# Kernel tuning notes

Measured on AMD Instinct MI355X. Metric: run time of the kernel, lower is better.

## Reference

```python
import jax, jax.numpy as jnp
import numpy as np

D_MODEL = 2048
N_HEADS = 16
HEAD_DIM = D_MODEL // N_HEADS
D_FF = 8192
B, T = 2, 2048
LN_EPS = 1e-5


def layer_norm(x, g, b):
    mu = jnp.mean(x, axis=-1, keepdims=True)
    var = jnp.mean(jnp.square(x - mu), axis=-1, keepdims=True)
    return (x - mu) * jax.lax.rsqrt(var + LN_EPS) * g + b


def setup_inputs() -> dict:
    key = jax.random.key(0)
    ks = jax.random.split(key, 8)
    s = 0.02
    return {
        "x": jax.random.normal(ks[0], (B, T, D_MODEL), dtype=jnp.float32),
        "ln1_g": jnp.ones((D_MODEL,), jnp.float32),
        "ln1_b": jnp.zeros((D_MODEL,), jnp.float32),
        "ln2_g": jnp.ones((D_MODEL,), jnp.float32),
        "ln2_b": jnp.zeros((D_MODEL,), jnp.float32),
        "w_qkv": jax.random.normal(ks[1], (3 * D_MODEL, D_MODEL), jnp.float32) * s,
        "w_out": jax.random.normal(ks[2], (D_MODEL, D_MODEL), jnp.float32) * s,
        "w_up": jax.random.normal(ks[3], (D_FF, D_MODEL), jnp.float32) * s,
        "b_up": jnp.zeros((D_FF,), jnp.float32),
        "w_down": jax.random.normal(ks[4], (D_MODEL, D_FF), jnp.float32) * s,
        "b_down": jnp.zeros((D_MODEL,), jnp.float32),
    }


def reference(x, ln1_g, ln1_b, ln2_g, ln2_b, w_qkv, w_out, w_up, b_up, w_down, b_down):
    b, t, c = x.shape
    # --- attention (pre-norm) ---
    h = layer_norm(x, ln1_g, ln1_b)
    qkv = h @ w_qkv.T                                  # [B,T,3C]
    q, k, v = jnp.split(qkv, 3, axis=-1)
    # [B,H,T,Dh]
    q = q.reshape(b, t, N_HEADS, HEAD_DIM).transpose(0, 2, 1, 3)
    k = k.reshape(b, t, N_HEADS, HEAD_DIM).transpose(0, 2, 1, 3)
    v = v.reshape(b, t, N_HEADS, HEAD_DIM).transpose(0, 2, 1, 3)
    scale = 1.0 / np.sqrt(HEAD_DIM).astype(np.float32)
    attn = jnp.einsum("bhqd,bhkd->bhqk", q, k) * scale
    causal = jnp.tril(jnp.ones((t, t), dtype=bool))
    attn = jnp.where(causal, attn, jnp.float32(-jnp.inf))
    attn = jax.nn.softmax(attn, axis=-1)
    out = jnp.einsum("bhqk,bhkd->bhqd", attn, v)
    out = out.transpose(0, 2, 1, 3).reshape(b, t, c)
    x = x + out @ w_out.T
    # --- FFN (pre-norm, GeLU exact) ---
    h = layer_norm(x, ln2_g, ln2_b)
    h = jax.nn.gelu(h @ w_up.T + b_up, approximate=False)
    x = x + h @ w_down.T + b_down
    return x
```

## Files before the change

kernel.cpp:

```cpp
#include <hip/hip_runtime.h>
#include <cstdint>
#include <cstddef>

using u16 = unsigned short;
typedef __attribute__((ext_vector_type(8))) __bf16 bf16x8;
typedef __attribute__((ext_vector_type(4))) float f32x4;

__device__ inline u16 f2bf(float f) {
  union { float f; unsigned u; } v; v.f = f;
  unsigned r = (v.u + 0x7fffu + ((v.u >> 16) & 1u)) >> 16;
  return (u16)r;
}

__device__ inline float bf2f(u16 u) {
  union { unsigned u; float f; } v; v.u = (unsigned)u << 16;
  return v.f;
}

#define GLDS(g, s) __builtin_amdgcn_global_load_lds( \
    (__attribute__((address_space(1))) void*)(g), \
    (__attribute__((address_space(3))) void*)(s), 16, 0, 0)

__global__ __launch_bounds__(256) void cvt_all(const float* __restrict__ a0,
                                               const float* __restrict__ a1,
                                               const float* __restrict__ a2,
                                               const float* __restrict__ a3,
                                               u16* __restrict__ o0, u16* __restrict__ o1,
                                               u16* __restrict__ o2, u16* __restrict__ o3) {
  int stride = gridDim.x * 256;
  for (int i = blockIdx.x * 256 + threadIdx.x; i < 6291456; i += stride) {
    const float* in; u16* out; int j = i;
    if (j < 1572864) { in = a0; out = o0; }
    else if ((j -= 1572864) < 524288) { in = a1; out = o1; }
    else if ((j -= 524288) < 2097152) { in = a2; out = o2; }
    else { j -= 2097152; in = a3; out = o3; }
    float4 v0 = *(const float4*)&in[(size_t)j * 8];
    float4 v1 = *(const float4*)&in[(size_t)j * 8 + 4];
    union { u16 u[8]; uint4 q; } pk;
    pk.u[0] = f2bf(v0.x); pk.u[1] = f2bf(v0.y); pk.u[2] = f2bf(v0.z); pk.u[3] = f2bf(v0.w);
    pk.u[4] = f2bf(v1.x); pk.u[5] = f2bf(v1.y); pk.u[6] = f2bf(v1.z); pk.u[7] = f2bf(v1.w);
    *(uint4*)&out[(size_t)j * 8] = pk.q;
  }
}

__global__ __launch_bounds__(256) void ln_bf16(const float* __restrict__ x,
                                               const float* __restrict__ g,
                                               const float* __restrict__ bsh,
                                               u16* __restrict__ out) {
  __shared__ float red[8];
  int tid = threadIdx.x;
  int lane = tid & 63, w = tid >> 6;
  size_t row = blockIdx.x;
  const float* xr = x + row * 2048;
  float4 v0 = *(const float4*)&xr[tid * 8];
  float4 v1 = *(const float4*)&xr[tid * 8 + 4];
  float s = v0.x + v0.y + v0.z + v0.w + v1.x + v1.y + v1.z + v1.w;
  float s2 = v0.x*v0.x + v0.y*v0.y + v0.z*v0.z + v0.w*v0.w
           + v1.x*v1.x + v1.y*v1.y + v1.z*v1.z + v1.w*v1.w;
#pragma unroll
  for (int m = 1; m < 64; m <<= 1) { s += __shfl_xor(s, m); s2 += __shfl_xor(s2, m); }
  if (lane == 0) { red[w] = s; red[w + 4] = s2; }
  __syncthreads();
  s = red[0] + red[1] + red[2] + red[3];
  s2 = red[4] + red[5] + red[6] + red[7];
  float mu = s * (1.0f / 2048.0f);
  float var = s2 * (1.0f / 2048.0f) - mu * mu;
  float rs = rsqrtf(var + 1e-5f);
  float4 g0 = *(const float4*)&g[tid * 8];
  float4 g1 = *(const float4*)&g[tid * 8 + 4];
  float4 b0 = *(const float4*)&bsh[tid * 8];
  float4 b1 = *(const float4*)&bsh[tid * 8 + 4];
  float xv[8] = {v0.x, v0.y, v0.z, v0.w, v1.x, v1.y, v1.z, v1.w};
  float gv[8] = {g0.x, g0.y, g0.z, g0.w, g1.x, g1.y, g1.z, g1.w};
  float bv[8] = {b0.x, b0.y, b0.z, b0.w, b1.x, b1.y, b1.z, b1.w};
  union { u16 u[8]; uint4 q; } pk;
#pragma unroll
  for (int j = 0; j < 8; j++) pk.u[j] = f2bf((xv[j] - mu) * rs * gv[j] + bv[j]);
  *(uint4*)&out[row * 2048 + tid * 8] = pk.q;
}

__global__ __launch_bounds__(256) void combineLN(const u16* __restrict__ p,
                                                 const float* __restrict__ resid,
                                                 const float* __restrict__ g,
                                                 const float* __restrict__ bsh,
                                                 float* __restrict__ x1,
                                                 u16* __restrict__ hb) {
  __shared__ float red[8];
  int tid = threadIdx.x, lane = tid & 63, w = tid >> 6;
  size_t row = blockIdx.x;
  size_t base = row * 2048 + tid * 8;
  union { uint4 q; u16 u[8]; } a, b;
  a.q = *(const uint4*)&p[base];
  b.q = *(const uint4*)&p[8388608 + base];
  float4 r0 = *(const float4*)&resid[base];
  float4 r1 = *(const float4*)&resid[base + 4];
  float v[8] = {r0.x, r0.y, r0.z, r0.w, r1.x, r1.y, r1.z, r1.w};
  float s = 0.f, s2 = 0.f;
#pragma unroll
  for (int j = 0; j < 8; ++j) {
    v[j] += bf2f(a.u[j]) + bf2f(b.u[j]);
    s += v[j]; s2 += v[j] * v[j];
  }
  *(float4*)&x1[base] = (float4){v[0], v[1], v[2], v[3]};
  *(float4*)&x1[base + 4] = (float4){v[4], v[5], v[6], v[7]};
#pragma unroll
  for (int m = 1; m < 64; m <<= 1) { s += __shfl_xor(s, m); s2 += __shfl_xor(s2, m); }
  if (lane == 0) { red[w] = s; red[w + 4] = s2; }
  __syncthreads();
  s = red[0] + red[1] + red[2] + red[3];
  s2 = red[4] + red[5] + red[6] + red[7];
  float mu = s * (1.0f / 2048.0f);
  float var = s2 * (1.0f / 2048.0f) - mu * mu;
  float rs = rsqrtf(var + 1e-5f);
  float4 g0 = *(const float4*)&g[tid * 8];
  float4 g1 = *(const float4*)&g[tid * 8 + 4];
  float4 b0 = *(const float4*)&bsh[tid * 8];
  float4 b1 = *(const float4*)&bsh[tid * 8 + 4];
  float gv[8] = {g0.x, g0.y, g0.z, g0.w, g1.x, g1.y, g1.z, g1.w};
  float bv[8] = {b0.x, b0.y, b0.z, b0.w, b1.x, b1.y, b1.z, b1.w};
  union { u16 u[8]; uint4 q; } pk;
#pragma unroll
  for (int j = 0; j < 8; j++) pk.u[j] = f2bf((v[j] - mu) * rs * gv[j] + bv[j]);
  *(uint4*)&hb[base] = pk.q;
}

__global__ __launch_bounds__(256) void combine2f(const u16* __restrict__ p,
                                                 const float* __restrict__ resid,
                                                 const float* __restrict__ bias,
                                                 float* __restrict__ out, int n8) {
  int stride = gridDim.x * 256;
  for (int i = blockIdx.x * 256 + threadIdx.x; i < n8; i += stride) {
    size_t base = (size_t)i * 8;
    union { uint4 q; u16 u[8]; } a, b;
    a.q = *(const uint4*)&p[base];
    b.q = *(const uint4*)&p[8388608 + base];
    float4 r0 = *(const float4*)&resid[base];
    float4 r1 = *(const float4*)&resid[base + 4];
    int col0 = (int)(base & 2047);
    float4 bb0 = *(const float4*)&bias[col0];
    float4 bb1 = *(const float4*)&bias[col0 + 4];
    float v[8] = {r0.x + bb0.x, r0.y + bb0.y, r0.z + bb0.z, r0.w + bb0.w,
                  r1.x + bb1.x, r1.y + bb1.y, r1.z + bb1.z, r1.w + bb1.w};
#pragma unroll
    for (int j = 0; j < 8; ++j) v[j] += bf2f(a.u[j]) + bf2f(b.u[j]);
    *(float4*)&out[base] = (float4){v[0], v[1], v[2], v[3]};
    *(float4*)&out[base + 4] = (float4){v[4], v[5], v[6], v[7]};
  }
}

template <int EPI, int LDK, int KLEN, int NSPLIT>
__global__ __launch_bounds__(512, 4) void gemm_bk32(
    const u16* __restrict__ A, const u16* __restrict__ B,
    int M, int N, const float* __restrict__ bias, u16* __restrict__ outh,
    int xc, int chr, int chc) {
  __shared__ u16 lds[36864];
  constexpr int NT = KLEN / 32;
  int tid = threadIdx.x;
  int lane = tid & 63, wid = tid >> 6;
  int wr = wid >> 2, wc = wid & 3;
  int lr = lane & 15, lg = lane >> 4;

  unsigned dly = (blockIdx.x * 2654435761u) >> 29;
  for (unsigned i = 0; i < dly; ++i) asm volatile("s_sleep 6" ::: "memory");

  int sub = blockIdx.x;
  if (NSPLIT > 1) {
    int per = (M >> 7) * (N >> 8);
    int ks = sub / per;
    sub -= ks * per;
    A += (size_t)ks * KLEN;
    B += (size_t)ks * KLEN;
    outh += (size_t)ks * M * N;
  }
  int xcd = sub & 7, slot = sub >> 3;
  int rr = slot / chc, cc = slot - rr * chc;
  int by = (xcd / xc) * chr + rr;
  int bx = (xcd - (xcd / xc) * xc) * chc + cc;
  size_t bm = (size_t)by * 128, bn = (size_t)bx * 256;

  const u16* Ablk = A + bm * LDK;
  const u16* Bblk = B + bn * LDK;

  int sA = (tid >> 2) * LDK + (((tid & 3) ^ ((tid >> 3) & 3)) * 8);
  int gs = (lg ^ ((lr >> 1) & 3)) * 8;
  int aoff = (wr * 64 + lr) * 32 + gs;
  int boff = 4096 + (wc * 64 + lr) * 32 + gs;

  f32x4 acc[4][4];
#pragma unroll
  for (int mq = 0; mq < 4; ++mq)
#pragma unroll
    for (int nq = 0; nq < 4; ++nq) acc[mq][nq] = (f32x4){0.f, 0.f, 0.f, 0.f};

  bf16x8 af[4], bfr[4];

#define STAGE(bb, tt) do { \
    const u16* As = Ablk + (tt) * 32 + sA; \
    const u16* Bs = Bblk + (tt) * 32 + sA; \
    GLDS(As, &lds[(bb) * 12288 + tid * 8]); \
    GLDS(Bs, &lds[(bb) * 12288 + 4096 + tid * 8]); \
    GLDS(Bs + 128 * (size_t)LDK, &lds[(bb) * 12288 + 8192 + tid * 8]); \
  } while (0)
#define BARS do { __builtin_amdgcn_s_barrier(); __builtin_amdgcn_sched_barrier(0); } while (0)

  STAGE(0, 0);
  STAGE(1, 1);

  int c = 0;
  for (int t = 0; t < NT; ++t) {
    if (t + 1 < NT) {
      asm volatile("s_waitcnt vmcnt(3)" ::: "memory");
    } else {
      asm volatile("s_waitcnt vmcnt(0)" ::: "memory");
    }
    BARS;
#pragma unroll
    for (int mq = 0; mq < 4; ++mq)
      af[mq] = *(const bf16x8*)&lds[c * 12288 + mq * 512 + aoff];
#pragma unroll
    for (int nq = 0; nq < 4; ++nq)
      bfr[nq] = *(const bf16x8*)&lds[c * 12288 + nq * 512 + boff];
    if (t + 2 < NT) {
      int cs = c + 2; if (cs >= 3) cs -= 3;
      STAGE(cs, t + 2);
    }
    __builtin_amdgcn_s_setprio(1);
#pragma unroll
    for (int mq = 0; mq < 4; ++mq)
#pragma unroll
      for (int nq = 0; nq < 4; ++nq)
        acc[mq][nq] = __builtin_amdgcn_mfma_f32_16x16x32_bf16(af[mq], bfr[nq], acc[mq][nq], 0, 0, 0);
    __builtin_amdgcn_s_setprio(0);
    c = (c == 2) ? 0 : c + 1;
  }

#undef STAGE
#undef BARS

  size_t row0 = bm + wr * 64, col0 = bn + wc * 64;
#pragma unroll
  for (int mq = 0; mq < 4; ++mq) {
#pragma unroll
    for (int nq = 0; nq < 4; ++nq) {
#pragma unroll
      for (int r = 0; r < 4; ++r) {
        size_t row = row0 + mq * 16 + lg * 4 + r;
        size_t col = col0 + nq * 16 + lr;
        size_t idx = row * (size_t)N + col;
        float v = acc[mq][nq][r];
        if (EPI == 0) {
          outh[idx] = f2bf(v);
        } else {
          v += bias[col];
          outh[idx] = f2bf(0.5f * v * (1.0f + erff(v * 0.70710678118654752f)));
        }
      }
    }
  }
}

__global__ __launch_bounds__(256) void vtrans(const u16* __restrict__ qkv,
                                              u16* __restrict__ vt) {
  __shared__ u16 tile[32][33];
  int tx = threadIdx.x & 31, ty = threadIdx.x >> 5;
  int t0 = blockIdx.x * 32, d0 = blockIdx.y * 32, bh = blockIdx.z;
  int b = bh >> 4, h = bh & 15;
  const u16* src = qkv + (size_t)b * 2048 * 6144 + 4096 + h * 128 + d0;
#pragma unroll
  for (int i = 0; i < 4; i++)
    tile[ty + i * 8][tx] = src[(size_t)(t0 + ty + i * 8) * 6144 + tx];
  __syncthreads();
  u16* dst = vt + (size_t)bh * 128 * 2048 + (size_t)d0 * 2048 + t0;
#pragma unroll
  for (int i = 0; i < 4; i++)
    dst[(size_t)(ty + i * 8) * 2048 + tx] = tile[tx][ty + i * 8];
}

__device__ inline void stage_kv(const u16* __restrict__ ktok, const u16* __restrict__ vbase,
                                int k0, u16* kb, u16* vb, int tid) {
#pragma unroll
  for (int c = 0; c < 4; ++c) {
    int s = c * 256 + tid;
    int r = s >> 4, g = s & 15;
    const u16* src = ktok + (size_t)(k0 + r) * 6144 + ((g ^ (r & 7)) * 8);
    GLDS(src, &kb[s * 8]);
  }
#pragma unroll
  for (int c = 0; c < 4; ++c) {
    int s = c * 256 + tid;
    int d = s >> 3, g = s & 7;
    const u16* src = vbase + (size_t)d * 2048 + k0 + ((g ^ (d & 7)) * 8);
    GLDS(src, &vb[s * 8]);
  }
}

__global__ __launch_bounds__(256) void attn_fwd(const u16* __restrict__ qkv,
                                                const u16* __restrict__ vt,
                                                u16* __restrict__ outh) {
  __shared__ u16 kbuf[2][8192];
  __shared__ u16 vbuf[2][8192];
  __shared__ u16 p_lds[4][1024];
  int tid = threadIdx.x, lane = tid & 63, w = tid >> 6;
  int lr = lane & 15, lg = lane >> 4;
  int bh = blockIdx.x, p = blockIdx.y;
  int b = bh >> 4, h = bh & 15;
  const float scale = 0.08838834764831845f;
  const u16* tokbase = qkv + (size_t)b * 2048 * 6144;
  const u16* ktok = tokbase + 2048 + h * 128;
  const u16* vbase = vt + (size_t)bh * 262144;
  u16* pl = p_lds[w];

  for (int half = 0; half < 2; ++half) {
    int qt = (half == 0) ? p : 31 - p;
    int qbase = qt * 64 + w * 16;
    int nt = qt + 1;

    bf16x8 qf[4];
    const u16* qrow_ptr = tokbase + (size_t)(qbase + lr) * 6144 + h * 128;
#pragma unroll
    for (int kk = 0; kk < 4; kk++) qf[kk] = *(const bf16x8*)&qrow_ptr[kk * 32 + lg * 8];

    f32x4 o[8];
#pragma unroll
    for (int d = 0; d < 8; d++) o[d] = (f32x4){0.f, 0.f, 0.f, 0.f};
    float mrow[4] = {-1e30f, -1e30f, -1e30f, -1e30f};
    float lsum[4] = {0.f, 0.f, 0.f, 0.f};

    int cur = 0;
    stage_kv(ktok, vbase, 0, kbuf[0], vbuf[0], tid);
    __syncthreads();

    for (int t = 0; t < nt; ++t) {
      int k0 = t * 64;
      if (t + 1 < nt) stage_kv(ktok, vbase, k0 + 64, kbuf[cur ^ 1], vbuf[cur ^ 1], tid);
      const u16* kb = kbuf[cur];
      const u16* vb = vbuf[cur];

      f32x4 s[4];
#pragma unroll
      for (int c = 0; c < 4; c++) s[c] = (f32x4){0.f, 0.f, 0.f, 0.f};
#pragma unroll
      for (int kk = 0; kk < 4; kk++) {
#pragma unroll
        for (int c = 0; c < 4; c++) {
          bf16x8 kf = *(const bf16x8*)&kb[(c * 16 + lr) * 128 + (((kk * 4 + lg) ^ (lr & 7)) * 8)];
          s[c] = __builtin_amdgcn_mfma_f32_16x16x32_bf16(qf[kk], kf, s[c], 0, 0, 0);
        }
      }

      float mt[4];
#pragma unroll
      for (int r = 0; r < 4; r++) {
        int qrow = qbase + lg * 4 + r;
        float m = -1e30f;
#pragma unroll
        for (int c = 0; c < 4; c++) {
          int key = k0 + c * 16 + lr;
          float v = (key <= qrow) ? s[c][r] * scale : -1e30f;
          s[c][r] = v;
          m = fmaxf(m, v);
        }
        mt[r] = m;
      }
#pragma unroll
      for (int msk = 1; msk < 16; msk <<= 1)
#pragma unroll
        for (int r = 0; r < 4; r++) mt[r] = fmaxf(mt[r], __shfl_xor(mt[r], msk));
      float al[4], ps[4];
#pragma unroll
      for (int r = 0; r < 4; r++) {
        float mn = fmaxf(mrow[r], mt[r]);
        al[r] = __expf(mrow[r] - mn);
        mrow[r] = mn;
        float sum = 0.f;
#pragma unroll
        for (int c = 0; c < 4; c++) {
          float pv = __expf(s[c][r] - mn);
          s[c][r] = pv;
          sum += pv;
        }
        ps[r] = sum;
      }
#pragma unroll
      for (int msk = 1; msk < 16; msk <<= 1)
#pragma unroll
        for (int r = 0; r < 4; r++) ps[r] += __shfl_xor(ps[r], msk);
#pragma unroll
      for (int r = 0; r < 4; r++) lsum[r] = lsum[r] * al[r] + ps[r];
#pragma unroll
      for (int d = 0; d < 8; d++)
#pragma unroll
        for (int r = 0; r < 4; r++) o[d][r] *= al[r];

#pragma unroll
      for (int r = 0; r < 4; r++) {
        int prow = lg * 4 + r;
#pragma unroll
        for (int c = 0; c < 4; c++) {
          int gw = (c * 2 + (lr >> 3)) ^ (prow & 7);
          pl[prow * 64 + gw * 8 + (lr & 7)] = f2bf(s[c][r]);
        }
      }
      asm volatile("s_waitcnt lgkmcnt(0)" ::: "memory");
      bf16x8 pa[2];
#pragma unroll
      for (int ks = 0; ks < 2; ks++)
        pa[ks] = *(const bf16x8*)&pl[lr * 64 + (((ks * 4 + lg) ^ (lr & 7)) * 8)];
#pragma unroll
      for (int dt = 0; dt < 8; dt++) {
#pragma unroll
        for (int ks = 0; ks < 2; ks++) {
          bf16x8 vf = *(const bf16x8*)&vb[(dt * 16 + lr) * 64 + (((ks * 4 + lg) ^ (lr & 7)) * 8)];
          o[dt] = __builtin_amdgcn_mfma_f32_16x16x32_bf16(pa[ks], vf, o[dt], 0, 0, 0);
        }
      }
      __syncthreads();
      cur ^= 1;
    }

    float inv[4];
#pragma unroll
    for (int r = 0; r < 4; r++) inv[r] = 1.0f / lsum[r];
    u16* ob = outh + (size_t)(b * 2048 + qbase) * 2048 + h * 128;
#pragma unroll
    for (int dt = 0; dt < 8; dt++)
#pragma unroll
      for (int r = 0; r < 4; r++)
        ob[(size_t)(lg * 4 + r) * 2048 + dt * 16 + lr] = f2bf(o[dt][r] * inv[r]);
  }
}

extern "C" void kernel_launch(void* const* d_in, const int* in_sizes, int n_in,
                              void* d_out, int out_size, void* d_ws, size_t ws_size,
                              hipStream_t stream) {
  const float* x      = (const float*)d_in[0];
  const float* ln1_g  = (const float*)d_in[1];
  const float* ln1_b  = (const float*)d_in[2];
  const float* ln2_g  = (const float*)d_in[3];
  const float* ln2_b  = (const float*)d_in[4];
  const float* w_qkv  = (const float*)d_in[5];
  const float* w_out  = (const float*)d_in[6];
  const float* w_up   = (const float*)d_in[7];
  const float* b_up   = (const float*)d_in[8];
  const float* w_down = (const float*)d_in[9];
  const float* b_down = (const float*)d_in[10];
  float* outp = (float*)d_out;

  char* ws = (char*)d_ws;
  u16* w_qkv_bf  = (u16*)(ws + 0);
  u16* w_out_bf  = (u16*)(ws + 25165824);
  u16* w_up_bf   = (u16*)(ws + 33554432);
  u16* w_down_bf = (u16*)(ws + 67108864);
  u16* hb        = (u16*)(ws + 100663296);
  u16* qkvb      = (u16*)(ws + 117440512);
  u16* vtb       = (u16*)(ws + 167772160);
  u16* ub        = (u16*)(ws + 117440512);
  float* x1      = (float*)(ws + 184549376);
  u16* oPartH    = (u16*)(ws + 117440512);
  u16* dPartH    = (u16*)(ws + 0);

  cvt_all<<<4096, 256, 0, stream>>>(w_qkv, w_out, w_up, w_down,
                                    w_qkv_bf, w_out_bf, w_up_bf, w_down_bf);

  ln_bf16<<<4096, 256, 0, stream>>>(x, ln1_g, ln1_b, hb);
  gemm_bk32<0, 2048, 2048, 1><<<768, 512, 0, stream>>>(hb, w_qkv_bf, 4096, 6144,
                                                       nullptr, qkvb, 4, 16, 6);
  vtrans<<<dim3(64, 4, 32), 256, 0, stream>>>(qkvb, vtb);
  attn_fwd<<<dim3(32, 16), 256, 0, stream>>>(qkvb, vtb, hb);
  gemm_bk32<0, 2048, 1024, 2><<<512, 512, 0, stream>>>(hb, w_out_bf, 4096, 2048,
                                                       nullptr, oPartH, 2, 8, 4);
  combineLN<<<4096, 256, 0, stream>>>(oPartH, x, ln2_g, ln2_b, x1, hb);

  gemm_bk32<2, 2048, 2048, 1><<<1024, 512, 0, stream>>>(hb, w_up_bf, 4096, 8192,
                                                        b_up, ub, 4, 16, 8);
  gemm_bk32<0, 8192, 4096, 2><<<512, 512, 0, stream>>>(ub, w_down_bf, 4096, 2048,
                                                       nullptr, dPartH, 2, 8, 4);
  combine2f<<<2048, 256, 0, stream>>>(dPartH, x1, b_down, outp, 1048576);
}
```

Before: 621.2 us.

## Fold weight conversions into LN and QKV GEMM kernels to drop standalone cvt pass

Removes the separate cvt_all kernel. The qkv and out-projection weight conversion now runs as a grid-stride tail in ln_bf16, and the up and down weight conversion as a tail in the QKV GEMM. This saves one launch and lets the conversion traffic overlap with other kernels' tails instead of serialising. The QKV GEMM takes on extra memory-bound work after its epilogue, which may lengthen it and compete for bandwidth.

```diff
diff --git a/kernel.cpp b/kernel.cpp
--- a/kernel.cpp
+++ b/kernel.cpp
@@ -17,36 +17,27 @@
   return v.f;
 }
 
+__device__ inline void cvt8(const float* __restrict__ in, u16* __restrict__ out, int j) {
+  float4 v0 = *(const float4*)&in[(size_t)j * 8];
+  float4 v1 = *(const float4*)&in[(size_t)j * 8 + 4];
+  union { u16 u[8]; uint4 q; } pk;
+  pk.u[0] = f2bf(v0.x); pk.u[1] = f2bf(v0.y); pk.u[2] = f2bf(v0.z); pk.u[3] = f2bf(v0.w);
+  pk.u[4] = f2bf(v1.x); pk.u[5] = f2bf(v1.y); pk.u[6] = f2bf(v1.z); pk.u[7] = f2bf(v1.w);
+  *(uint4*)&out[(size_t)j * 8] = pk.q;
+}
+
 #define GLDS(g, s) __builtin_amdgcn_global_load_lds( \
     (__attribute__((address_space(1))) void*)(g), \
     (__attribute__((address_space(3))) void*)(s), 16, 0, 0)
 
-__global__ __launch_bounds__(256) void cvt_all(const float* __restrict__ a0,
-                                               const float* __restrict__ a1,
-                                               const float* __restrict__ a2,
-                                               const float* __restrict__ a3,
-                                               u16* __restrict__ o0, u16* __restrict__ o1,
-                                               u16* __restrict__ o2, u16* __restrict__ o3) {
-  int stride = gridDim.x * 256;
-  for (int i = blockIdx.x * 256 + threadIdx.x; i < 6291456; i += stride) {
-    const float* in; u16* out; int j = i;
-    if (j < 1572864) { in = a0; out = o0; }
-    else if ((j -= 1572864) < 524288) { in = a1; out = o1; }
-    else if ((j -= 524288) < 2097152) { in = a2; out = o2; }
-    else { j -= 2097152; in = a3; out = o3; }
-    float4 v0 = *(const float4*)&in[(size_t)j * 8];
-    float4 v1 = *(const float4*)&in[(size_t)j * 8 + 4];
-    union { u16 u[8]; uint4 q; } pk;
-    pk.u[0] = f2bf(v0.x); pk.u[1] = f2bf(v0.y); pk.u[2] = f2bf(v0.z); pk.u[3] = f2bf(v0.w);
-    pk.u[4] = f2bf(v1.x); pk.u[5] = f2bf(v1.y); pk.u[6] = f2bf(v1.z); pk.u[7] = f2bf(v1.w);
-    *(uint4*)&out[(size_t)j * 8] = pk.q;
-  }
-}
-
 __global__ __launch_bounds__(256) void ln_bf16(const float* __restrict__ x,
                                                const float* __restrict__ g,
                                                const float* __restrict__ bsh,
-                                               u16* __restrict__ out) {
+                                               u16* __restrict__ out,
+                                               const float* __restrict__ wq,
+                                               const float* __restrict__ wo,
+                                               u16* __restrict__ wqh,
+                                               u16* __restrict__ woh) {
   __shared__ float red[8];
   int tid = threadIdx.x;
   int lane = tid & 63, w = tid >> 6;
@@ -77,6 +68,11 @@
 #pragma unroll
   for (int j = 0; j < 8; j++) pk.u[j] = f2bf((xv[j] - mu) * rs * gv[j] + bv[j]);
   *(uint4*)&out[row * 2048 + tid * 8] = pk.q;
+  int stride = gridDim.x * 256;
+  for (int i = blockIdx.x * 256 + tid; i < 2097152; i += stride) {
+    if (i < 1572864) cvt8(wq, wqh, i);
+    else cvt8(wo, woh, i - 1572864);
+  }
 }
 
 __global__ __launch_bounds__(256) void combineLN(const u16* __restrict__ p,
@@ -148,11 +144,13 @@
   }
 }
 
-template <int EPI, int LDK, int KLEN, int NSPLIT>
+template <int EPI, int LDK, int KLEN, int NSPLIT, bool CVT>
 __global__ __launch_bounds__(512, 4) void gemm_bk32(
     const u16* __restrict__ A, const u16* __restrict__ B,
     int M, int N, const float* __restrict__ bias, u16* __restrict__ outh,
-    int xc, int chr, int chc) {
+    int xc, int chr, int chc,
+    const float* __restrict__ cv0, const float* __restrict__ cv1,
+    u16* __restrict__ cd0, u16* __restrict__ cd1) {
   __shared__ u16 lds[36864];
   constexpr int NT = KLEN / 32;
   int tid = threadIdx.x;
@@ -255,6 +253,14 @@
           outh[idx] = f2bf(0.5f * v * (1.0f + erff(v * 0.70710678118654752f)));
         }
       }
+    }
+  }
+
+  if (CVT) {
+    int stride = gridDim.x * 512;
+    for (int i = blockIdx.x * 512 + tid; i < 4194304; i += stride) {
+      if (i < 2097152) cvt8(cv0, cd0, i);
+      else cvt8(cv1, cd1, i - 2097152);
     }
   }
 }
@@ -459,21 +465,23 @@
   u16* oPartH    = (u16*)(ws + 117440512);
   u16* dPartH    = (u16*)(ws + 0);
 
-  cvt_all<<<4096, 256, 0, stream>>>(w_qkv, w_out, w_up, w_down,
-                                    w_qkv_bf, w_out_bf, w_up_bf, w_down_bf);
-
-  ln_bf16<<<4096, 256, 0, stream>>>(x, ln1_g, ln1_b, hb);
-  gemm_bk32<0, 2048, 2048, 1><<<768, 512, 0, stream>>>(hb, w_qkv_bf, 4096, 6144,
-                                                       nullptr, qkvb, 4, 16, 6);
+  ln_bf16<<<4096, 256, 0, stream>>>(x, ln1_g, ln1_b, hb,
+                                    w_qkv, w_out, w_qkv_bf, w_out_bf);
+  gemm_bk32<0, 2048, 2048, 1, true><<<768, 512, 0, stream>>>(
+      hb, w_qkv_bf, 4096, 6144, nullptr, qkvb, 4, 16, 6,
+      w_up, w_down, w_up_bf, w_down_bf);
   vtrans<<<dim3(64, 4, 32), 256, 0, stream>>>(qkvb, vtb);
   attn_fwd<<<dim3(32, 16), 256, 0, stream>>>(qkvb, vtb, hb);
-  gemm_bk32<0, 2048, 1024, 2><<<512, 512, 0, stream>>>(hb, w_out_bf, 4096, 2048,
-                                                       nullptr, oPartH, 2, 8, 4);
+  gemm_bk32<0, 2048, 1024, 2, false><<<512, 512, 0, stream>>>(
+      hb, w_out_bf, 4096, 2048, nullptr, oPartH, 2, 8, 4,
+      nullptr, nullptr, nullptr, nullptr);
   combineLN<<<4096, 256, 0, stream>>>(oPartH, x, ln2_g, ln2_b, x1, hb);
 
-  gemm_bk32<2, 2048, 2048, 1><<<1024, 512, 0, stream>>>(hb, w_up_bf, 4096, 8192,
-                                                        b_up, ub, 4, 16, 8);
-  gemm_bk32<0, 8192, 4096, 2><<<512, 512, 0, stream>>>(ub, w_down_bf, 4096, 2048,
-                                                       nullptr, dPartH, 2, 8, 4);
+  gemm_bk32<2, 2048, 2048, 1, false><<<1024, 512, 0, stream>>>(
+      hb, w_up_bf, 4096, 8192, b_up, ub, 4, 16, 8,
+      nullptr, nullptr, nullptr, nullptr);
+  gemm_bk32<0, 8192, 4096, 2, false><<<512, 512, 0, stream>>>(
+      ub, w_down_bf, 4096, 2048, nullptr, dPartH, 2, 8, 4,
+      nullptr, nullptr, nullptr, nullptr);
   combine2f<<<2048, 256, 0, stream>>>(dPartH, x1, b_down, outp, 1048576);
 }
```

After: 622.3 us. No clear change (+0.2%).

## Double-buffer LDS fragment reads and deepen GEMM prefetch to three stages

Applied to the files above, without the earlier changes.

Restructures the GEMM main loop so that LDS fragments for the next K-tile are read into a second register set while MFMAs run on the current set, and the global-to-LDS prefetch is issued three tiles ahead instead of two. The loop is manually unrolled by two so it can alternate between the A and B register sets. The aim is to hide LDS read latency behind MFMA work. In exchange it uses more VGPRs, which may lower occupancy, and it relies on NT being handled correctly at odd tails and on the reuse of the 3-slot LDS ring being safe.

```diff
diff --git a/kernel.cpp b/kernel.cpp
--- a/kernel.cpp
+++ b/kernel.cpp
@@ -192,7 +192,7 @@
 #pragma unroll
     for (int nq = 0; nq < 4; ++nq) acc[mq][nq] = (f32x4){0.f, 0.f, 0.f, 0.f};
 
-  bf16x8 af[4], bfr[4];
+  bf16x8 afA[4], bfA[4], afB[4], bfB[4];
 
 #define STAGE(bb, tt) do { \
     const u16* As = Ablk + (tt) * 32 + sA; \
@@ -201,41 +201,53 @@
     GLDS(Bs, &lds[(bb) * 12288 + 4096 + tid * 8]); \
     GLDS(Bs + 128 * (size_t)LDK, &lds[(bb) * 12288 + 8192 + tid * 8]); \
   } while (0)
+#define READF(sl, AF, BF) do { \
+    _Pragma("unroll") for (int mq = 0; mq < 4; ++mq) \
+      AF[mq] = *(const bf16x8*)&lds[(sl) * 12288 + mq * 512 + aoff]; \
+    _Pragma("unroll") for (int nq = 0; nq < 4; ++nq) \
+      BF[nq] = *(const bf16x8*)&lds[(sl) * 12288 + nq * 512 + boff]; \
+  } while (0)
+#define MFMAF(AF, BF) do { \
+    __builtin_amdgcn_s_setprio(1); \
+    _Pragma("unroll") for (int mq = 0; mq < 4; ++mq) \
+    _Pragma("unroll") for (int nq = 0; nq < 4; ++nq) \
+      acc[mq][nq] = __builtin_amdgcn_mfma_f32_16x16x32_bf16(AF[mq], BF[nq], acc[mq][nq], 0, 0, 0); \
+    __builtin_amdgcn_s_setprio(0); \
+  } while (0)
 #define BARS do { __builtin_amdgcn_s_barrier(); __builtin_amdgcn_sched_barrier(0); } while (0)
-
-  STAGE(0, 0);
-  STAGE(1, 1);
+#define VM3 asm volatile("s_waitcnt vmcnt(3)" ::: "memory")
+#define VM0 asm volatile("s_waitcnt vmcnt(0)" ::: "memory")
+
+  STAGE(0, 0); STAGE(1, 1); STAGE(2, 2);
+  asm volatile("s_waitcnt vmcnt(6)" ::: "memory");
+  BARS;
+  READF(0, afA, bfA);
 
   int c = 0;
-  for (int t = 0; t < NT; ++t) {
-    if (t + 1 < NT) {
-      asm volatile("s_waitcnt vmcnt(3)" ::: "memory");
-    } else {
-      asm volatile("s_waitcnt vmcnt(0)" ::: "memory");
-    }
+  for (int t = 0; t < NT; t += 2) {
+    if (t + 3 <= NT) { VM3; } else { VM0; }
     BARS;
-#pragma unroll
-    for (int mq = 0; mq < 4; ++mq)
-      af[mq] = *(const bf16x8*)&lds[c * 12288 + mq * 512 + aoff];
-#pragma unroll
-    for (int nq = 0; nq < 4; ++nq)
-      bfr[nq] = *(const bf16x8*)&lds[c * 12288 + nq * 512 + boff];
-    if (t + 2 < NT) {
-      int cs = c + 2; if (cs >= 3) cs -= 3;
-      STAGE(cs, t + 2);
-    }
-    __builtin_amdgcn_s_setprio(1);
-#pragma unroll
-    for (int mq = 0; mq < 4; ++mq)
-#pragma unroll
-      for (int nq = 0; nq < 4; ++nq)
-        acc[mq][nq] = __builtin_amdgcn_mfma_f32_16x16x32_bf16(af[mq], bfr[nq], acc[mq][nq], 0, 0, 0);
-    __builtin_amdgcn_s_setprio(0);
-    c = (c == 2) ? 0 : c + 1;
+    if (t + 3 < NT) STAGE(c, t + 3);
+    int cn = c + 1; if (cn == 3) cn = 0;
+    if (t + 1 < NT) READF(cn, afB, bfB);
+    MFMAF(afA, bfA);
+    c = cn;
+    int t1 = t + 1;
+    if (t1 + 3 <= NT) { VM3; } else { VM0; }
+    BARS;
+    if (t1 + 3 < NT) STAGE(c, t1 + 3);
+    int cn2 = c + 1; if (cn2 == 3) cn2 = 0;
+    if (t1 + 1 < NT) READF(cn2, afA, bfA);
+    MFMAF(afB, bfB);
+    c = cn2;
   }
 
 #undef STAGE
+#undef READF
+#undef MFMAF
 #undef BARS
+#undef VM3
+#undef VM0
 
   size_t row0 = bm + wr * 64, col0 = bn + wc * 64;
 #pragma unroll
```

New measurement: 1.712 ms. +175.6%, slower.
